# Kernel tuning notes

Hardware: AMD Instinct MI355X
Metric: run time of the kernel (lower is better)

Reference implementation:

```python
import jax, jax.numpy as jnp
import numpy as np

N_QUBITS = 4
N_LAYERS = 3
N_FEATURES = 64
BATCH = 524288


def setup_inputs() -> dict:
    key = jax.random.key(0)
    k1, k2, k3, k4 = jax.random.split(key, 4)
    x = jax.random.normal(k1, (BATCH, N_FEATURES), jnp.float32)
    # nn.Linear(64, 4) params
    lim = 1.0 / np.sqrt(N_FEATURES)
    W_pre = jax.random.uniform(k2, (N_QUBITS, N_FEATURES), jnp.float32, -lim, lim)
    b_pre = jax.random.uniform(k3, (N_QUBITS,), jnp.float32, -lim, lim)
    # quantum circuit weights: randn * 0.1
    qweights = jax.random.normal(k4, (N_LAYERS, N_QUBITS, 2), jnp.float32) * 0.1
    return {"x": x, "W_pre": W_pre, "b_pre": b_pre, "qweights": qweights}


def _coef(theta, n):
    # reshape scalar or [B] angle to broadcast against [B, 2,..,2] (n-1 trailing dims after slicing)
    return jnp.reshape(theta, (-1,) + (1,) * (n - 1))


def _apply_ry(state, wire, theta):
    # RY(t) = [[cos t/2, -sin t/2], [sin t/2, cos t/2]] applied on `wire`
    n = state.ndim - 1
    s = jnp.moveaxis(state, 1 + wire, -1)
    a, b = s[..., 0], s[..., 1]
    c = _coef(jnp.cos(theta / 2), n)
    sn = _coef(jnp.sin(theta / 2), n)
    out = jnp.stack([c * a - sn * b, sn * a + c * b], axis=-1)
    return jnp.moveaxis(out, -1, 1 + wire)


def _apply_rz(state, wire, theta):
    # RZ(t) = diag(e^{-i t/2}, e^{+i t/2})
    n = state.ndim - 1
    s = jnp.moveaxis(state, 1 + wire, -1)
    half = _coef(theta / 2, n)
    out = jnp.stack([jnp.exp(-1j * half) * s[..., 0],
                     jnp.exp(1j * half) * s[..., 1]], axis=-1)
    return jnp.moveaxis(out, -1, 1 + wire)


def _apply_cnot(state, ctrl, tgt):
    s = jnp.moveaxis(state, (1 + ctrl, 1 + tgt), (-2, -1))
    s = jnp.concatenate([s[..., 0:1, :], s[..., 1:2, ::-1]], axis=-2)
    return jnp.moveaxis(s, (-2, -1), (1 + ctrl, 1 + tgt))


def _circuit(angles, qweights):
    # batched 4-qubit statevector simulation; state shape [B, 2,2,2,2] (wire 0 = MSB)
    B, n = angles.shape
    nl = qweights.shape[0]
    state = jnp.zeros((B,) + (2,) * n, jnp.complex64)
    state = state.at[(slice(None),) + (0,) * n].set(1.0)
    for w in range(n):
        state = _apply_ry(state, w, angles[:, w])
    for l in range(nl):
        for w in range(n):
            state = _apply_ry(state, w, qweights[l, w, 0])
            state = _apply_rz(state, w, qweights[l, w, 1])
        for w in range(n):
            state = _apply_cnot(state, w, (w + 1) % n)
    probs = state.real ** 2 + state.imag ** 2  # [B, 2,2,2,2] float32
    exps = []
    for w in range(n):
        marg = jnp.moveaxis(probs, 1 + w, 1).reshape(B, 2, -1).sum(-1)  # [B, 2]
        exps.append(marg[:, 0] - marg[:, 1])  # <Z_w>
    return jnp.stack(exps, axis=1)  # [B, n]


def reference(x, W_pre, b_pre, qweights):
    angles = jnp.tanh(x @ W_pre.T + b_pre)  # [B, n_qubits]
    return _circuit(angles, qweights).astype(jnp.float32)
```

## Files before the change

kernel.cpp:

```cpp
#include <hip/hip_runtime.h>
#include <cmath>


typedef __attribute__((ext_vector_type(8))) short bf16x8;
typedef __attribute__((ext_vector_type(4))) float f32x4;

__device__ __forceinline__ short f2bf(float f) {
  const unsigned u = __float_as_uint(f);
  return (short)((u + 0x7FFF + ((u >> 16) & 1)) >> 16);
}

__global__ __launch_bounds__(256) void qprep_kernel(
    const float* __restrict__ qw,
    float* __restrict__ A_out)
{
  __shared__ float sre[16][17];
  __shared__ float sim[16][17];
  __shared__ float M[4][16][16];
  const int tid = threadIdx.x;
  const int col = tid >> 4;
  const int u   = tid & 15;

  sre[col][u] = (u == col) ? 1.0f : 0.0f;
  sim[col][u] = 0.0f;
  __syncthreads();

#pragma unroll
  for (int l = 0; l < 3; ++l) {
#pragma unroll
    for (int w = 0; w < 4; ++w) {
      const int mask = 8 >> w;
      float sh, ch, sh2, ch2;
      __sincosf(0.5f * qw[(l * 4 + w) * 2 + 0], &sh, &ch);
      __sincosf(0.5f * qw[(l * 4 + w) * 2 + 1], &sh2, &ch2);
      const int ua = u & ~mask, ub = u | mask;
      const float ar = sre[col][ua], ai = sim[col][ua];
      const float br = sre[col][ub], bi = sim[col][ub];
      __syncthreads();
      float nr, ni;
      if (u & mask) { nr = sh * ar + ch * br; ni = sh * ai + ch * bi; }
      else          { nr = ch * ar - sh * br; ni = ch * ai - sh * bi; }
      float rr, ri;
      if (u & mask) { rr = ch2 * nr - sh2 * ni; ri = ch2 * ni + sh2 * nr; }
      else          { rr = ch2 * nr + sh2 * ni; ri = ch2 * ni - sh2 * nr; }
      sre[col][u] = rr; sim[col][u] = ri;
      __syncthreads();
    }
    int src = u;
    if (src & 1) src ^= 8;
    if (src & 2) src ^= 1;
    if (src & 4) src ^= 2;
    if (src & 8) src ^= 4;
    const float pr = sre[col][src], pi = sim[col][src];
    __syncthreads();
    sre[col][u] = pr; sim[col][u] = pi;
    __syncthreads();
  }

  for (int idx = tid; idx < 1024; idx += 256) {
    const int w = idx >> 8, s = (idx >> 4) & 15, t = idx & 15;
    const int mask = 8 >> w;
    float acc = 0.0f;
#pragma unroll
    for (int uu = 0; uu < 16; ++uu) {
      const float z = (uu & mask) ? -1.0f : 1.0f;
      acc += z * (sre[s][uu] * sre[t][uu] + sim[s][uu] * sim[t][uu]);
    }
    M[w][s][t] = acc;
  }
  __syncthreads();

  for (int idx = tid; idx < 324; idx += 256) {
    const int w = idx & 3, pq = idx >> 2;
    const int p = pq / 9, q = pq % 9;
    const int i0 = p / 3, i1 = p % 3, i2 = q / 3, i3 = q % 3;
    float acc = 0.0f;
#pragma unroll
    for (int comb = 0; comb < 16; ++comb) {
      int s = 0, t = 0;
      float coef = 0.0625f;
      int j;
      j = (comb >> 3) & 1; s |= j << 3; t |= ((i0 == 2) ? (j ^ 1) : j) << 3; if (i0 == 1 && j) coef = -coef;
      j = (comb >> 2) & 1; s |= j << 2; t |= ((i1 == 2) ? (j ^ 1) : j) << 2; if (i1 == 1 && j) coef = -coef;
      j = (comb >> 1) & 1; s |= j << 1; t |= ((i2 == 2) ? (j ^ 1) : j) << 1; if (i2 == 1 && j) coef = -coef;
      j = comb & 1;        s |= j;      t |= ((i3 == 2) ? (j ^ 1) : j);      if (i3 == 1 && j) coef = -coef;
      acc = fmaf(coef, M[w][s][t], acc);
    }
    A_out[idx] = acc;
  }
}

#define LDSUB(V0, V1, V2, V3, R0, M) {                                      \
  const float* rp_ = x + ((R0) + (size_t)((M) * 16 + arow)) * 64 + kgrp * 8;\
  V0 = *reinterpret_cast<const float4*>(rp_);                               \
  V1 = *reinterpret_cast<const float4*>(rp_ + 4);                          \
  V2 = *reinterpret_cast<const float4*>(rp_ + 32);                         \
  V3 = *reinterpret_cast<const float4*>(rp_ + 36); }

#define DOMFMA(V0, V1, V2, V3, M) {                                         \
  bf16x8 af0_, af1_;                                                        \
  af0_[0] = f2bf(V0.x); af0_[1] = f2bf(V0.y); af0_[2] = f2bf(V0.z);         \
  af0_[3] = f2bf(V0.w); af0_[4] = f2bf(V1.x); af0_[5] = f2bf(V1.y);         \
  af0_[6] = f2bf(V1.z); af0_[7] = f2bf(V1.w);                               \
  af1_[0] = f2bf(V2.x); af1_[1] = f2bf(V2.y); af1_[2] = f2bf(V2.z);         \
  af1_[3] = f2bf(V2.w); af1_[4] = f2bf(V3.x); af1_[5] = f2bf(V3.y);         \
  af1_[6] = f2bf(V3.z); af1_[7] = f2bf(V3.w);                               \
  f32x4 acc_ = __builtin_amdgcn_mfma_f32_16x16x32_bf16(af0_, wf0, zero, 0, 0, 0); \
  acc_ = __builtin_amdgcn_mfma_f32_16x16x32_bf16(af1_, wf1, acc_, 0, 0, 0); \
  if (arow < 4) {                                                           \
    _Pragma("unroll")                                                       \
    for (int r_ = 0; r_ < 4; ++r_)                                          \
      myld[((M) * 16 + kgrp * 4 + r_) * 4 + arow] = acc_[r_];               \
  } }

#define TAIL(R0) {                                                          \
  asm volatile("" ::: "memory");                                            \
  const float4 ang = *reinterpret_cast<const float4*>(&myld[lane * 4]);     \
  const float t0 = 1.0f - 2.0f / (__expf(2.0f * (ang.x + bp[0])) + 1.0f);   \
  const float t1 = 1.0f - 2.0f / (__expf(2.0f * (ang.y + bp[1])) + 1.0f);   \
  const float t2 = 1.0f - 2.0f / (__expf(2.0f * (ang.z + bp[2])) + 1.0f);   \
  const float t3 = 1.0f - 2.0f / (__expf(2.0f * (ang.w + bp[3])) + 1.0f);   \
  float c0, s0, c1, s1, c2, s2, c3, s3;                                     \
  __sincosf(t0, &s0, &c0); __sincosf(t1, &s1, &c1);                         \
  __sincosf(t2, &s2, &c2); __sincosf(t3, &s3, &c3);                         \
  const float g[9] = {1.f, c1, s1, c0, c0 * c1, c0 * s1,                    \
                      s0, s0 * c1, s0 * s1};                                \
  const float h[9] = {1.f, c3, s3, c2, c2 * c3, c2 * s3,                    \
                      s2, s2 * c3, s2 * s3};                                \
  float e0 = 0.f, e1 = 0.f, e2 = 0.f, e3 = 0.f;                             \
  _Pragma("unroll")                                                         \
  for (int p_ = 0; p_ < 9; ++p_) {                                          \
    _Pragma("unroll")                                                       \
    for (int q_ = 0; q_ < 9; ++q_) {                                        \
      const float4 a4 = Aws[p_ * 9 + q_];                                   \
      const float tt = g[p_] * h[q_];                                       \
      e0 = fmaf(a4.x, tt, e0); e1 = fmaf(a4.y, tt, e1);                     \
      e2 = fmaf(a4.z, tt, e2); e3 = fmaf(a4.w, tt, e3);                     \
    }                                                                       \
  }                                                                         \
  reinterpret_cast<float4*>(out)[(R0) + lane] =                             \
      make_float4(e0, e1, e2, e3);                                          \
  asm volatile("" ::: "memory"); }

__global__ __launch_bounds__(256)
__attribute__((amdgpu_waves_per_eu(4, 4)))
void qmain_kernel(
    const float* __restrict__ x,
    const float* __restrict__ Wp,
    const float* __restrict__ bp,
    const float4* __restrict__ Aws,
    float* __restrict__ out)
{
  __shared__ float wlds[4][256];

  const int tid  = threadIdx.x;
  const int lane = tid & 63;
  const int wid  = tid >> 6;
  const int arow = lane & 15;
  const int kgrp = lane >> 4;
  float* myld = wlds[wid];

  const size_t wrow0 = ((size_t)blockIdx.x * 4 + wid) * 128;

  bf16x8 wf0, wf1;
#pragma unroll
  for (int j = 0; j < 8; ++j) {
    if (arow < 4) {
      wf0[j] = f2bf(Wp[arow * 64 + 0  + kgrp * 8 + j]);
      wf1[j] = f2bf(Wp[arow * 64 + 32 + kgrp * 8 + j]);
    } else {
      wf0[j] = 0; wf1[j] = 0;
    }
  }
  const f32x4 zero = {0.f, 0.f, 0.f, 0.f};

  const size_t r0 = wrow0;
  const size_t r1 = wrow0 + 64;

  float4 ua0, ua1, ua2, ua3, ub0, ub1, ub2, ub3;

  LDSUB(ua0, ua1, ua2, ua3, r0, 0);
  LDSUB(ub0, ub1, ub2, ub3, r0, 1);
  DOMFMA(ua0, ua1, ua2, ua3, 0); LDSUB(ua0, ua1, ua2, ua3, r0, 2);
  DOMFMA(ub0, ub1, ub2, ub3, 1); LDSUB(ub0, ub1, ub2, ub3, r0, 3);
  DOMFMA(ua0, ua1, ua2, ua3, 2); LDSUB(ua0, ua1, ua2, ua3, r1, 0);
  DOMFMA(ub0, ub1, ub2, ub3, 3);

  TAIL(r0);

  LDSUB(ub0, ub1, ub2, ub3, r1, 1);
  DOMFMA(ua0, ua1, ua2, ua3, 0); LDSUB(ua0, ua1, ua2, ua3, r1, 2);
  DOMFMA(ub0, ub1, ub2, ub3, 1); LDSUB(ub0, ub1, ub2, ub3, r1, 3);
  DOMFMA(ua0, ua1, ua2, ua3, 2);
  DOMFMA(ub0, ub1, ub2, ub3, 3);

  TAIL(r1);
}

extern "C" void kernel_launch(void* const* d_in, const int* in_sizes, int n_in,
                              void* d_out, int out_size, void* d_ws, size_t ws_size,
                              hipStream_t stream) {
  const float* x  = (const float*)d_in[0];
  const float* Wp = (const float*)d_in[1];
  const float* bp = (const float*)d_in[2];
  const float* qw = (const float*)d_in[3];
  float* out = (float*)d_out;
  float* A = (float*)d_ws;
  (void)n_in; (void)out_size; (void)ws_size;

  qprep_kernel<<<1, 256, 0, stream>>>(qw, A);

  const int B = in_sizes[0] / 64;
  qmain_kernel<<<B / 512, 256, 0, stream>>>(x, Wp, bp,
                                            (const float4*)A, out);
}
```

Measured before the change: 37.38 us.

## Deepen load prefetch to four sub-tiles with double-buffered LDS angles

Raises register prefetch depth from two to four 16-row sub-tiles of x per wave, so all loads for the second 64-row chunk are issued before the first chunk's tanh/expectation tail runs. The per-wave LDS scratch is split into two halves so the second chunk's MFMA results cannot overwrite angles the first tail is still reading. An explicit lgkmcnt wait plus a sched_barrier is added before the tail, and the waves-per-EU minimum is lowered to 3 to allow the extra 16 float4 registers. The aim is to hide global memory latency behind the tail compute, at the cost of higher register pressure and possibly lower occupancy.

```diff
diff --git a/kernel.cpp b/kernel.cpp
--- a/kernel.cpp
+++ b/kernel.cpp
@@ -90,14 +90,14 @@
   }
 }
 
-#define LDSUB(V0, V1, V2, V3, R0, M) {                                      \
-  const float* rp_ = x + ((R0) + (size_t)((M) * 16 + arow)) * 64 + kgrp * 8;\
+#define LDSUB(V0, V1, V2, V3, R0, S) {                                      \
+  const float* rp_ = x + ((R0) + (size_t)((S) * 16 + arow)) * 64 + kgrp * 8;\
   V0 = *reinterpret_cast<const float4*>(rp_);                               \
-  V1 = *reinterpret_cast<const float4*>(rp_ + 4);                          \
-  V2 = *reinterpret_cast<const float4*>(rp_ + 32);                         \
+  V1 = *reinterpret_cast<const float4*>(rp_ + 4);                           \
+  V2 = *reinterpret_cast<const float4*>(rp_ + 32);                          \
   V3 = *reinterpret_cast<const float4*>(rp_ + 36); }
 
-#define DOMFMA(V0, V1, V2, V3, M) {                                         \
+#define DOMFMA(V0, V1, V2, V3, M, LB) {                                     \
   bf16x8 af0_, af1_;                                                        \
   af0_[0] = f2bf(V0.x); af0_[1] = f2bf(V0.y); af0_[2] = f2bf(V0.z);         \
   af0_[3] = f2bf(V0.w); af0_[4] = f2bf(V1.x); af0_[5] = f2bf(V1.y);         \
@@ -110,12 +110,14 @@
   if (arow < 4) {                                                           \
     _Pragma("unroll")                                                       \
     for (int r_ = 0; r_ < 4; ++r_)                                          \
-      myld[((M) * 16 + kgrp * 4 + r_) * 4 + arow] = acc_[r_];               \
+      myld[(LB) * 256 + ((M) * 16 + kgrp * 4 + r_) * 4 + arow] = acc_[r_];  \
   } }
 
-#define TAIL(R0) {                                                          \
-  asm volatile("" ::: "memory");                                            \
-  const float4 ang = *reinterpret_cast<const float4*>(&myld[lane * 4]);     \
+#define TAIL(R0, LB) {                                                      \
+  asm volatile("s_waitcnt lgkmcnt(0)" ::: "memory");                        \
+  __builtin_amdgcn_sched_barrier(0);                                        \
+  const float4 ang =                                                        \
+      *reinterpret_cast<const float4*>(&myld[(LB) * 256 + lane * 4]);       \
   const float t0 = 1.0f - 2.0f / (__expf(2.0f * (ang.x + bp[0])) + 1.0f);   \
   const float t1 = 1.0f - 2.0f / (__expf(2.0f * (ang.y + bp[1])) + 1.0f);   \
   const float t2 = 1.0f - 2.0f / (__expf(2.0f * (ang.z + bp[2])) + 1.0f);   \
@@ -143,7 +145,7 @@
   asm volatile("" ::: "memory"); }
 
 __global__ __launch_bounds__(256)
-__attribute__((amdgpu_waves_per_eu(4, 4)))
+__attribute__((amdgpu_waves_per_eu(3, 4)))
 void qmain_kernel(
     const float* __restrict__ x,
     const float* __restrict__ Wp,
@@ -151,14 +153,14 @@
     const float4* __restrict__ Aws,
     float* __restrict__ out)
 {
-  __shared__ float wlds[4][256];
+  __shared__ alignas(16) float wlds[4][2][256];
 
   const int tid  = threadIdx.x;
   const int lane = tid & 63;
   const int wid  = tid >> 6;
   const int arow = lane & 15;
   const int kgrp = lane >> 4;
-  float* myld = wlds[wid];
+  float* myld = &wlds[wid][0][0];
 
   const size_t wrow0 = ((size_t)blockIdx.x * 4 + wid) * 128;
 
@@ -177,24 +179,26 @@
   const size_t r0 = wrow0;
   const size_t r1 = wrow0 + 64;
 
-  float4 ua0, ua1, ua2, ua3, ub0, ub1, ub2, ub3;
-
-  LDSUB(ua0, ua1, ua2, ua3, r0, 0);
-  LDSUB(ub0, ub1, ub2, ub3, r0, 1);
-  DOMFMA(ua0, ua1, ua2, ua3, 0); LDSUB(ua0, ua1, ua2, ua3, r0, 2);
-  DOMFMA(ub0, ub1, ub2, ub3, 1); LDSUB(ub0, ub1, ub2, ub3, r0, 3);
-  DOMFMA(ua0, ua1, ua2, ua3, 2); LDSUB(ua0, ua1, ua2, ua3, r1, 0);
-  DOMFMA(ub0, ub1, ub2, ub3, 3);
-
-  TAIL(r0);
-
-  LDSUB(ub0, ub1, ub2, ub3, r1, 1);
-  DOMFMA(ua0, ua1, ua2, ua3, 0); LDSUB(ua0, ua1, ua2, ua3, r1, 2);
-  DOMFMA(ub0, ub1, ub2, ub3, 1); LDSUB(ub0, ub1, ub2, ub3, r1, 3);
-  DOMFMA(ua0, ua1, ua2, ua3, 2);
-  DOMFMA(ub0, ub1, ub2, ub3, 3);
-
-  TAIL(r1);
+  float4 a0, a1, a2, a3, b0, b1, b2, b3;
+  float4 c0, c1, c2, c3, d0, d1, d2, d3;
+
+  LDSUB(a0, a1, a2, a3, r0, 0);
+  LDSUB(b0, b1, b2, b3, r0, 1);
+  LDSUB(c0, c1, c2, c3, r0, 2);
+  LDSUB(d0, d1, d2, d3, r0, 3);
+  DOMFMA(a0, a1, a2, a3, 0, 0); LDSUB(a0, a1, a2, a3, r1, 0);
+  DOMFMA(b0, b1, b2, b3, 1, 0); LDSUB(b0, b1, b2, b3, r1, 1);
+  DOMFMA(c0, c1, c2, c3, 2, 0); LDSUB(c0, c1, c2, c3, r1, 2);
+  DOMFMA(d0, d1, d2, d3, 3, 0); LDSUB(d0, d1, d2, d3, r1, 3);
+
+  TAIL(r0, 0);
+
+  DOMFMA(a0, a1, a2, a3, 0, 1);
+  DOMFMA(b0, b1, b2, b3, 1, 1);
+  DOMFMA(c0, c1, c2, c3, 2, 1);
+  DOMFMA(d0, d1, d2, d3, 3, 1);
+
+  TAIL(r1, 1);
 }
 
 extern "C" void kernel_launch(void* const* d_in, const int* in_sizes, int n_in,
```

New measurement: 35.81 us. 4.2% less time.
